# Optimization experiments

Hardware: AMD Instinct MI355X
Metric: run time of the kernel (lower is better)

## Reference

```python
import jax, jax.numpy as jnp
import numpy as np

EMBED_DIM = 768
NUM_HEADS = 12
MAX_LEN = 512
BATCH = 8
SEQ = 512
HEAD_DIM = EMBED_DIM // NUM_HEADS


def setup_inputs() -> dict:
    key = jax.random.key(0)
    ks = jax.random.split(key, 7)
    x = jax.random.normal(ks[0], (BATCH, SEQ, EMBED_DIM), dtype=jnp.float32)
    mask = jnp.ones((BATCH, SEQ), dtype=jnp.int32)
    Wq = jax.random.normal(ks[1], (EMBED_DIM, EMBED_DIM), dtype=jnp.float32) * (1.0 / np.sqrt(EMBED_DIM))
    Wk = jax.random.normal(ks[2], (EMBED_DIM, EMBED_DIM), dtype=jnp.float32) * (1.0 / np.sqrt(EMBED_DIM))
    Wv = jax.random.normal(ks[3], (EMBED_DIM, EMBED_DIM), dtype=jnp.float32) * (1.0 / np.sqrt(EMBED_DIM))
    rel_pos = jax.random.normal(ks[4], (2 * MAX_LEN - 1, NUM_HEADS), dtype=jnp.float32)
    Wo = jax.random.normal(ks[5], (EMBED_DIM, EMBED_DIM), dtype=jnp.float32) * (1.0 / np.sqrt(EMBED_DIM))
    bo = jax.random.normal(ks[6], (EMBED_DIM,), dtype=jnp.float32) * 0.02
    return {"x": x, "mask": mask, "Wq": Wq, "Wk": Wk, "Wv": Wv,
            "rel_pos": rel_pos, "Wo": Wo, "bo": bo}


def reference(x, mask, Wq, Wk, Wv, rel_pos, Wo, bo):
    B, S, E = x.shape
    H, D = NUM_HEADS, HEAD_DIM
    Q = (x @ Wq).reshape(B, S, H, D)
    K = (x @ Wk).reshape(B, S, H, D)
    V = (x @ Wv).reshape(B, S, H, D)
    # scores: [B, H, S, S]
    scores = jnp.einsum('bqhd,bkhd->bhqk', Q, K) / np.sqrt(D).astype(np.float32)
    # relative position bias: idx[q,k] = k - q + max_len - 1, clamped
    pos = jnp.arange(S)
    idx = jnp.clip(pos[None, :] - pos[:, None] + MAX_LEN - 1, 0, 2 * MAX_LEN - 2)
    bias = rel_pos[idx]                       # [S, S, H]
    scores = scores + jnp.transpose(bias, (2, 0, 1))[None]  # [1,H,S,S]
    # mask: b i * b j -> [B,1,S,S]
    m2 = (mask[:, None, :, None] * mask[:, None, None, :]) != 0
    mask_value = -jnp.finfo(scores.dtype).max
    scores = jnp.where(m2, scores, mask_value)
    attn = jax.nn.softmax(scores, axis=-1)
    out = jnp.einsum('bhqk,bkhd->bqhd', attn, V).reshape(B, S, E)
    out = out @ Wo + bo  # dropout is identity in eval mode
    return out
```

## Files before the change

kernel.cpp:

```cpp
#include <hip/hip_runtime.h>
#include <hip/hip_bf16.h>
#include <cfloat>
#include <cstdint>
#include <cmath>

#define EMBED 768
#define NHEAD 12
#define SEQB  8
#define SEQ   512
#define HDIM  64
#define WMAT  589824

typedef __attribute__((ext_vector_type(8))) short short8;
typedef __attribute__((ext_vector_type(4))) short short4v;
typedef __attribute__((ext_vector_type(4))) float f32x4;

__device__ __forceinline__ short f2bf(float f) {
  uint32_t u = __float_as_uint(f);
  u += 0x7FFF + ((u >> 16) & 1u);
  return (short)(u >> 16);
}

__device__ __forceinline__ short f2bf1(float f) {
  int r;
  asm("v_cvt_pk_bf16_f32 %0, %1, %2" : "=v"(r) : "v"(f), "v"(f));
  return (short)r;
}

__device__ __forceinline__ void gload_lds16(const void* g, void* l) {
  __builtin_amdgcn_global_load_lds((const __attribute__((address_space(1))) void*)g,
                                   (__attribute__((address_space(3))) void*)l, 16, 0, 0);
}

__global__ void k_cast_x(const float* __restrict__ x, short* __restrict__ xb) {
  int i = blockIdx.x * blockDim.x + threadIdx.x;
  const int n4 = SEQB * SEQ * EMBED / 4;
  if (i < n4) {
    float4 v = ((const float4*)x)[i];
    short4v o;
    o.x = f2bf(v.x); o.y = f2bf(v.y); o.z = f2bf(v.z); o.w = f2bf(v.w);
    ((short4v*)xb)[i] = o;
  }
}

__global__ void k_cast_wt(const float* __restrict__ Wq, const float* __restrict__ Wk,
                          const float* __restrict__ Wv, const float* __restrict__ Wo,
                          short* __restrict__ Wt) {
  __shared__ float tile[32][33];
  const int mat = blockIdx.z;
  const float* src = (mat == 0) ? Wq : (mat == 1) ? Wk : (mat == 2) ? Wv : Wo;
  const int n0 = blockIdx.x * 32, k0 = blockIdx.y * 32;
  const int tx = threadIdx.x & 31, ty = threadIdx.x >> 5;
  #pragma unroll
  for (int rr = 0; rr < 4; rr++)
    tile[ty + rr * 8][tx] = src[(size_t)(k0 + ty + rr * 8) * EMBED + n0 + tx];
  __syncthreads();
  short* dst = Wt + (size_t)mat * WMAT;
  #pragma unroll
  for (int rr = 0; rr < 4; rr++)
    dst[(size_t)(n0 + ty + rr * 8) * EMBED + k0 + tx] = f2bf(tile[tx][ty + rr * 8]);
}

template <int MODE>
__launch_bounds__(256)
__global__ void k_gemm(const short* __restrict__ A, const short* __restrict__ B,
                       short* __restrict__ O0, short* __restrict__ O1,
                       short* __restrict__ O2,
                       float* __restrict__ OF, const float* __restrict__ bias) {
  __shared__ __attribute__((aligned(16))) short As[2][128 * 32];
  __shared__ __attribute__((aligned(16))) short Bs[2][128 * 32];
  const int tid = threadIdx.x;
  const int lane = tid & 63, w = tid >> 6;
  const int g = lane >> 4, c = lane & 15;
  const int wi = (w >> 1) * 64, wj = (w & 1) * 64;
  const int i0 = blockIdx.y * 128, j0 = blockIdx.x * 128;
  const int NSTEP = EMBED / 32;

  f32x4 acc[4][4];
  #pragma unroll
  for (int a = 0; a < 4; a++)
    #pragma unroll
    for (int b2 = 0; b2 < 4; b2++) acc[a][b2] = (f32x4){0.f, 0.f, 0.f, 0.f};

  #define GSTAGE(S, BUF)                                                            \
    { _Pragma("unroll")                                                             \
      for (int it = 0; it < 2; it++) {                                              \
        int gi = tid + it * 256;                                                    \
        int row = gi >> 2, qq = gi & 3;                                             \
        gload_lds16(A + (size_t)(i0 + row) * EMBED + (S) * 32 + qq * 8,             \
                    &As[BUF][gi * 8]);                                              \
        gload_lds16(B + (size_t)(j0 + row) * EMBED + (S) * 32 + qq * 8,             \
                    &Bs[BUF][gi * 8]);                                              \
      } }

  GSTAGE(0, 0)
  __syncthreads();

  for (int s = 0; s < NSTEP; ++s) {
    const int cur = s & 1;
    if (s < NSTEP - 1) {
      GSTAGE(s + 1, cur ^ 1)
      asm volatile("s_waitcnt vmcnt(4)" ::: "memory");
    } else {
      asm volatile("s_waitcnt vmcnt(0)" ::: "memory");
    }
    __builtin_amdgcn_sched_barrier(0);
    __builtin_amdgcn_s_barrier();
    __builtin_amdgcn_sched_barrier(0);

    short8 aF[4], bF[4];
    #pragma unroll
    for (int mi = 0; mi < 4; mi++) aF[mi] = *(const short8*)&As[cur][(wi + mi * 16 + c) * 32 + g * 8];
    #pragma unroll
    for (int nj = 0; nj < 4; nj++) bF[nj] = *(const short8*)&Bs[cur][(wj + nj * 16 + c) * 32 + g * 8];
    #pragma unroll
    for (int mi = 0; mi < 4; mi++)
      #pragma unroll
      for (int nj = 0; nj < 4; nj++)
        acc[mi][nj] = __builtin_amdgcn_mfma_f32_16x16x32_bf16(aF[mi], bF[nj], acc[mi][nj], 0, 0, 0);

    __builtin_amdgcn_s_barrier();
    __builtin_amdgcn_sched_barrier(0);
  }

  #pragma unroll
  for (int mi = 0; mi < 4; mi++) {
    int i = i0 + wi + mi * 16 + 4 * g;
    #pragma unroll
    for (int nj = 0; nj < 4; nj++) {
      int j = j0 + wj + nj * 16 + c;
      f32x4 v = acc[mi][nj];
      if (MODE == 0) {
        int n = i, m = j;
        int b = m >> 9, s = m & 511;
        if (n < 1536) {
          short* dst = O0; int nn = n;
          if (n >= 768) { dst = O1; nn -= 768; }
          int h = nn >> 6, d = nn & 63;
          short4v o; o.x = f2bf(v.x); o.y = f2bf(v.y); o.z = f2bf(v.z); o.w = f2bf(v.w);
          *(short4v*)&dst[(size_t)(((b * 12 + h) * 512 + s) * 64 + d)] = o;
        } else {
          int nn = n - 1536;
          int h = nn >> 6, d = nn & 63;
          size_t base = ((size_t)(b * 12 + h) * 64 + d) * 512 + s;
          O2[base] = f2bf(v.x); O2[base + 512] = f2bf(v.y);
          O2[base + 1024] = f2bf(v.z); O2[base + 1536] = f2bf(v.w);
        }
      } else {
        int n = i, m = j;
        float4 bb = *(const float4*)&bias[n];
        float4 o; o.x = v.x + bb.x; o.y = v.y + bb.y; o.z = v.z + bb.z; o.w = v.w + bb.w;
        *(float4*)&OF[(size_t)m * EMBED + n] = o;
      }
    }
  }
}

__launch_bounds__(256)
__global__ void k_attn(const short* __restrict__ Q, const short* __restrict__ K,
                       const short* __restrict__ Vt, const int* __restrict__ mask,
                       const float* __restrict__ rel_pos, short* __restrict__ attO) {
  __shared__ float bias_lds[1024];
  __shared__ int mask_lds[512];
  __shared__ __attribute__((aligned(16))) short Plds[4][16 * 32];
  __shared__ __attribute__((aligned(16))) short Kbuf[2][32 * 64];
  __shared__ __attribute__((aligned(16))) short Vbuf[2][64 * 32];
  const int tid = threadIdx.x;
  const int lane = tid & 63, w = tid >> 6;
  const int g = lane >> 4, c = lane & 15;
  const int bid = blockIdx.x;
  const int q0 = (bid / 96) * 64;
  const int bh = bid % 96;
  const int b = bh / 12, h = bh % 12;
  const short* Qb = Q + (size_t)bh * (512 * 64);
  const short* Kb = K + (size_t)bh * (512 * 64);
  const short* Vb = Vt + (size_t)bh * (64 * 512);

  const float LOG2E = 1.44269504089f;
  for (int i = tid; i < 1023; i += 256) bias_lds[i] = (rel_pos[i * 12 + h] - 16.0f) * LOG2E;
  for (int i = tid; i < 512; i += 256) mask_lds[i] = mask[b * 512 + i];

  const int krow_s = tid >> 3, kc_s = tid & 7;
  const int vrow_s = tid >> 2, vc_s = tid & 3;
  #define STAGEKV(T, BUF)                                                             \
    {                                                                                 \
      gload_lds16(Kb + ((T) * 32 + krow_s) * 64 + (kc_s ^ (krow_s & 7)) * 8,          \
                  &Kbuf[BUF][tid * 8]);                                               \
      gload_lds16(Vb + (size_t)vrow_s * 512 + (T) * 32 + (vc_s ^ ((vrow_s >> 1) & 3)) * 8, \
                  &Vbuf[BUF][tid * 8]);                                               \
    }

  STAGEKV(0, 0)

  short8 qf[2];
  #pragma unroll
  for (int dc = 0; dc < 2; dc++)
    qf[dc] = *(const short8*)&Qb[(q0 + w * 16 + c) * 64 + dc * 32 + g * 8];

  __syncthreads();

  int qrow[4], mq[4], bbase[4];
  #pragma unroll
  for (int r = 0; r < 4; r++) {
    qrow[r] = q0 + w * 16 + 4 * g + r;
    mq[r] = mask_lds[qrow[r]];
    bbase[r] = 511 - qrow[r];
  }

  float l_part[4];
  f32x4 accO[4];
  #pragma unroll
  for (int r = 0; r < 4; r++) l_part[r] = 0.f;
  #pragma unroll
  for (int dt = 0; dt < 4; dt++) accO[dt] = (f32x4){0.f, 0.f, 0.f, 0.f};

  const float SC = 0.125f * 1.44269504089f;
  short* Pw = &Plds[w][0];
  const int rdoff = c * 32 + g * 8;
  const int kswz = c & 7;
  const int vswz = (c >> 1) & 3;

  for (int t = 0; t < 16; ++t) {
    const int cur = t & 1;
    if (t < 15) {
      STAGEKV(t + 1, cur ^ 1)
      asm volatile("s_waitcnt vmcnt(2)" ::: "memory");
    } else {
      asm volatile("s_waitcnt vmcnt(0)" ::: "memory");
    }
    __builtin_amdgcn_sched_barrier(0);
    __builtin_amdgcn_s_barrier();
    __builtin_amdgcn_sched_barrier(0);

    const short* Kt = &Kbuf[cur][0];
    const short* Vs = &Vbuf[cur][0];

    short8 kf[4], vf[4];
    #pragma unroll
    for (int ct = 0; ct < 2; ct++)
      #pragma unroll
      for (int dc = 0; dc < 2; dc++)
        kf[ct * 2 + dc] = *(const short8*)&Kt[(ct * 16 + c) * 64 + ((dc * 4 + g) ^ kswz) * 8];
    #pragma unroll
    for (int dt = 0; dt < 4; dt++)
      vf[dt] = *(const short8*)&Vs[(dt * 16 + c) * 32 + ((g ^ vswz)) * 8];

    f32x4 s0 = (f32x4){0.f, 0.f, 0.f, 0.f}, s1 = s0;
    s0 = __builtin_amdgcn_mfma_f32_16x16x32_bf16(qf[0], kf[0], s0, 0, 0, 0);
    s0 = __builtin_amdgcn_mfma_f32_16x16x32_bf16(qf[1], kf[1], s0, 0, 0, 0);
    s1 = __builtin_amdgcn_mfma_f32_16x16x32_bf16(qf[0], kf[2], s1, 0, 0, 0);
    s1 = __builtin_amdgcn_mfma_f32_16x16x32_bf16(qf[1], kf[3], s1, 0, 0, 0);

    float p_[2][4];
    {
      const int krow = t * 32 + c;
      const int mk0 = mask_lds[krow], mk1 = mask_lds[krow + 16];
      #pragma unroll
      for (int r = 0; r < 4; r++) {
        float a0 = fmaf(s0[r], SC, bias_lds[krow + bbase[r]]);
        float a1 = fmaf(s1[r], SC, bias_lds[krow + 16 + bbase[r]]);
        float p0 = exp2f(a0), p1 = exp2f(a1);
        if ((mq[r] & mk0) == 0) p0 = 0.f;
        if ((mq[r] & mk1) == 0) p1 = 0.f;
        p_[0][r] = p0; p_[1][r] = p1;
        l_part[r] += p0 + p1;
      }
    }
    #pragma unroll
    for (int ct = 0; ct < 2; ct++)
      #pragma unroll
      for (int r = 0; r < 4; r++)
        Pw[(4 * g + r) * 32 + ct * 16 + c] = f2bf1(p_[ct][r]);
    short8 pa = *(const short8*)&Pw[rdoff];
    #pragma unroll
    for (int dt = 0; dt < 4; dt++)
      accO[dt] = __builtin_amdgcn_mfma_f32_16x16x32_bf16(pa, vf[dt], accO[dt], 0, 0, 0);

    __builtin_amdgcn_s_barrier();
    __builtin_amdgcn_sched_barrier(0);
  }

  float inv[4];
  #pragma unroll
  for (int r = 0; r < 4; r++) {
    float lr = l_part[r];
    #pragma unroll
    for (int off = 1; off < 16; off <<= 1) lr += __shfl_xor(lr, off);
    inv[r] = 1.0f / lr;
  }
  #pragma unroll
  for (int dt = 0; dt < 4; dt++)
    #pragma unroll
    for (int r = 0; r < 4; r++)
      attO[(size_t)(b * 512 + qrow[r]) * EMBED + h * 64 + dt * 16 + c] =
          f2bf(accO[dt][r] * inv[r]);
}

extern "C" void kernel_launch(void* const* d_in, const int* in_sizes, int n_in,
                              void* d_out, int out_size, void* d_ws, size_t ws_size,
                              hipStream_t stream) {
  const float* x = (const float*)d_in[0];
  const int* mask = (const int*)d_in[1];
  const float* Wq = (const float*)d_in[2];
  const float* Wk = (const float*)d_in[3];
  const float* Wv = (const float*)d_in[4];
  const float* rel_pos = (const float*)d_in[5];
  const float* Wo = (const float*)d_in[6];
  const float* bo = (const float*)d_in[7];
  float* out = (float*)d_out;

  char* ws = (char*)d_ws;
  short* xb = (short*)ws;
  short* Wt = (short*)(ws + 6291456);
  short* Qg = (short*)(ws + 6291456 + 4718592);
  short* Kg = Qg + 3145728;
  short* Vt = Kg + 3145728;
  short* attO = xb;

  k_cast_x<<<3072, 256, 0, stream>>>(x, xb);
  k_cast_wt<<<dim3(24, 24, 4), 256, 0, stream>>>(Wq, Wk, Wv, Wo, Wt);
  k_gemm<0><<<dim3(32, 18), 256, 0, stream>>>(Wt, xb, Qg, Kg, Vt, nullptr, nullptr);
  k_attn<<<768, 256, 0, stream>>>(Qg, Kg, Vt, mask, rel_pos, attO);
  k_gemm<2><<<dim3(32, 6), 256, 0, stream>>>(Wt + 3 * WMAT, attO, nullptr, nullptr, nullptr, out, bo);
}
```

Before: 155.6 us.

## Fuse cast kernels, triple-buffer GEMM stages, widen attention KV tiles

```diff
diff --git a/kernel.cpp b/kernel.cpp
--- a/kernel.cpp
+++ b/kernel.cpp
@@ -32,33 +32,32 @@
                                    (__attribute__((address_space(3))) void*)l, 16, 0, 0);
 }
 
-__global__ void k_cast_x(const float* __restrict__ x, short* __restrict__ xb) {
-  int i = blockIdx.x * blockDim.x + threadIdx.x;
-  const int n4 = SEQB * SEQ * EMBED / 4;
-  if (i < n4) {
+__global__ void k_cast(const float* __restrict__ x,
+                       const float* __restrict__ Wq, const float* __restrict__ Wk,
+                       const float* __restrict__ Wv, const float* __restrict__ Wo,
+                       short* __restrict__ xb, short* __restrict__ Wt) {
+  __shared__ float tile[32][33];
+  const int bx = blockIdx.x;
+  if (bx < 2304) {
+    const int mat = bx / 576, rem = bx % 576;
+    const float* src = (mat == 0) ? Wq : (mat == 1) ? Wk : (mat == 2) ? Wv : Wo;
+    const int n0 = (rem % 24) * 32, k0 = (rem / 24) * 32;
+    const int tx = threadIdx.x & 31, ty = threadIdx.x >> 5;
+    #pragma unroll
+    for (int rr = 0; rr < 4; rr++)
+      tile[ty + rr * 8][tx] = src[(size_t)(k0 + ty + rr * 8) * EMBED + n0 + tx];
+    __syncthreads();
+    short* dst = Wt + (size_t)mat * WMAT;
+    #pragma unroll
+    for (int rr = 0; rr < 4; rr++)
+      dst[(size_t)(n0 + ty + rr * 8) * EMBED + k0 + tx] = f2bf(tile[tx][ty + rr * 8]);
+  } else {
+    int i = (bx - 2304) * 256 + threadIdx.x;
     float4 v = ((const float4*)x)[i];
     short4v o;
     o.x = f2bf(v.x); o.y = f2bf(v.y); o.z = f2bf(v.z); o.w = f2bf(v.w);
     ((short4v*)xb)[i] = o;
   }
-}
-
-__global__ void k_cast_wt(const float* __restrict__ Wq, const float* __restrict__ Wk,
-                          const float* __restrict__ Wv, const float* __restrict__ Wo,
-                          short* __restrict__ Wt) {
-  __shared__ float tile[32][33];
-  const int mat = blockIdx.z;
-  const float* src = (mat == 0) ? Wq : (mat == 1) ? Wk : (mat == 2) ? Wv : Wo;
-  const int n0 = blockIdx.x * 32, k0 = blockIdx.y * 32;
-  const int tx = threadIdx.x & 31, ty = threadIdx.x >> 5;
-  #pragma unroll
-  for (int rr = 0; rr < 4; rr++)
-    tile[ty + rr * 8][tx] = src[(size_t)(k0 + ty + rr * 8) * EMBED + n0 + tx];
-  __syncthreads();
-  short* dst = Wt + (size_t)mat * WMAT;
-  #pragma unroll
-  for (int rr = 0; rr < 4; rr++)
-    dst[(size_t)(n0 + ty + rr * 8) * EMBED + k0 + tx] = f2bf(tile[tx][ty + rr * 8]);
 }
 
 template <int MODE>
@@ -67,8 +66,8 @@
                        short* __restrict__ O0, short* __restrict__ O1,
                        short* __restrict__ O2,
                        float* __restrict__ OF, const float* __restrict__ bias) {
-  __shared__ __attribute__((aligned(16))) short As[2][128 * 32];
-  __shared__ __attribute__((aligned(16))) short Bs[2][128 * 32];
+  __shared__ __attribute__((aligned(16))) short As[3][128 * 32];
+  __shared__ __attribute__((aligned(16))) short Bs[3][128 * 32];
   const int tid = threadIdx.x;
   const int lane = tid & 63, w = tid >> 6;
   const int g = lane >> 4, c = lane & 15;
@@ -94,12 +93,14 @@
       } }
 
   GSTAGE(0, 0)
-  __syncthreads();
+  GSTAGE(1, 1)
 
   for (int s = 0; s < NSTEP; ++s) {
-    const int cur = s & 1;
-    if (s < NSTEP - 1) {
-      GSTAGE(s + 1, cur ^ 1)
+    const int cur = s % 3;
+    if (s + 2 < NSTEP) {
+      GSTAGE(s + 2, (s + 2) % 3)
+      asm volatile("s_waitcnt vmcnt(8)" ::: "memory");
+    } else if (s + 1 < NSTEP) {
       asm volatile("s_waitcnt vmcnt(4)" ::: "memory");
     } else {
       asm volatile("s_waitcnt vmcnt(0)" ::: "memory");
@@ -162,9 +163,9 @@
                        const float* __restrict__ rel_pos, short* __restrict__ attO) {
   __shared__ float bias_lds[1024];
   __shared__ int mask_lds[512];
-  __shared__ __attribute__((aligned(16))) short Plds[4][16 * 32];
-  __shared__ __attribute__((aligned(16))) short Kbuf[2][32 * 64];
-  __shared__ __attribute__((aligned(16))) short Vbuf[2][64 * 32];
+  __shared__ __attribute__((aligned(16))) short Plds[4][16 * 64];
+  __shared__ __attribute__((aligned(16))) short Kbuf[2][64 * 64];
+  __shared__ __attribute__((aligned(16))) short Vbuf[2][64 * 64];
   const int tid = threadIdx.x;
   const int lane = tid & 63, w = tid >> 6;
   const int g = lane >> 4, c = lane & 15;
@@ -180,15 +181,16 @@
   for (int i = tid; i < 1023; i += 256) bias_lds[i] = (rel_pos[i * 12 + h] - 16.0f) * LOG2E;
   for (int i = tid; i < 512; i += 256) mask_lds[i] = mask[b * 512 + i];
 
-  const int krow_s = tid >> 3, kc_s = tid & 7;
-  const int vrow_s = tid >> 2, vc_s = tid & 3;
   #define STAGEKV(T, BUF)                                                             \
-    {                                                                                 \
-      gload_lds16(Kb + ((T) * 32 + krow_s) * 64 + (kc_s ^ (krow_s & 7)) * 8,          \
-                  &Kbuf[BUF][tid * 8]);                                               \
-      gload_lds16(Vb + (size_t)vrow_s * 512 + (T) * 32 + (vc_s ^ ((vrow_s >> 1) & 3)) * 8, \
-                  &Vbuf[BUF][tid * 8]);                                               \
-    }
+    { _Pragma("unroll")                                                               \
+      for (int it = 0; it < 2; it++) {                                                \
+        int gi = tid + it * 256;                                                      \
+        int row = gi >> 3, ch = gi & 7;                                               \
+        gload_lds16(Kb + ((T) * 64 + row) * 64 + (ch ^ (row & 7)) * 8,                \
+                    &Kbuf[BUF][gi * 8]);                                              \
+        gload_lds16(Vb + (size_t)row * 512 + (T) * 64 + (ch ^ (row & 7)) * 8,         \
+                    &Vbuf[BUF][gi * 8]);                                              \
+      } }
 
   STAGEKV(0, 0)
 
@@ -216,15 +218,13 @@
 
   const float SC = 0.125f * 1.44269504089f;
   short* Pw = &Plds[w][0];
-  const int rdoff = c * 32 + g * 8;
-  const int kswz = c & 7;
-  const int vswz = (c >> 1) & 3;
-
-  for (int t = 0; t < 16; ++t) {
+  const int cswz = c & 7;
+
+  for (int t = 0; t < 8; ++t) {
     const int cur = t & 1;
-    if (t < 15) {
+    if (t < 7) {
       STAGEKV(t + 1, cur ^ 1)
-      asm volatile("s_waitcnt vmcnt(2)" ::: "memory");
+      asm volatile("s_waitcnt vmcnt(4)" ::: "memory");
     } else {
       asm volatile("s_waitcnt vmcnt(0)" ::: "memory");
     }
@@ -235,46 +235,44 @@
     const short* Kt = &Kbuf[cur][0];
     const short* Vs = &Vbuf[cur][0];
 
-    short8 kf[4], vf[4];
-    #pragma unroll
-    for (int ct = 0; ct < 2; ct++)
-      #pragma unroll
-      for (int dc = 0; dc < 2; dc++)
-        kf[ct * 2 + dc] = *(const short8*)&Kt[(ct * 16 + c) * 64 + ((dc * 4 + g) ^ kswz) * 8];
-    #pragma unroll
-    for (int dt = 0; dt < 4; dt++)
-      vf[dt] = *(const short8*)&Vs[(dt * 16 + c) * 32 + ((g ^ vswz)) * 8];
-
-    f32x4 s0 = (f32x4){0.f, 0.f, 0.f, 0.f}, s1 = s0;
-    s0 = __builtin_amdgcn_mfma_f32_16x16x32_bf16(qf[0], kf[0], s0, 0, 0, 0);
-    s0 = __builtin_amdgcn_mfma_f32_16x16x32_bf16(qf[1], kf[1], s0, 0, 0, 0);
-    s1 = __builtin_amdgcn_mfma_f32_16x16x32_bf16(qf[0], kf[2], s1, 0, 0, 0);
-    s1 = __builtin_amdgcn_mfma_f32_16x16x32_bf16(qf[1], kf[3], s1, 0, 0, 0);
-
-    float p_[2][4];
-    {
-      const int krow = t * 32 + c;
-      const int mk0 = mask_lds[krow], mk1 = mask_lds[krow + 16];
+    f32x4 s4[4];
+    #pragma unroll
+    for (int ct = 0; ct < 4; ct++) {
+      short8 kf0 = *(const short8*)&Kt[(ct * 16 + c) * 64 + ((0 + g) ^ cswz) * 8];
+      short8 kf1 = *(const short8*)&Kt[(ct * 16 + c) * 64 + ((4 + g) ^ cswz) * 8];
+      f32x4 s = (f32x4){0.f, 0.f, 0.f, 0.f};
+      s = __builtin_amdgcn_mfma_f32_16x16x32_bf16(qf[0], kf0, s, 0, 0, 0);
+      s = __builtin_amdgcn_mfma_f32_16x16x32_bf16(qf[1], kf1, s, 0, 0, 0);
+      s4[ct] = s;
+    }
+
+    #pragma unroll
+    for (int ct = 0; ct < 4; ct++) {
+      const int krow = t * 64 + ct * 16 + c;
+      const int mk = mask_lds[krow];
+      float p_[4];
       #pragma unroll
       for (int r = 0; r < 4; r++) {
-        float a0 = fmaf(s0[r], SC, bias_lds[krow + bbase[r]]);
-        float a1 = fmaf(s1[r], SC, bias_lds[krow + 16 + bbase[r]]);
-        float p0 = exp2f(a0), p1 = exp2f(a1);
-        if ((mq[r] & mk0) == 0) p0 = 0.f;
-        if ((mq[r] & mk1) == 0) p1 = 0.f;
-        p_[0][r] = p0; p_[1][r] = p1;
-        l_part[r] += p0 + p1;
+        float a0 = fmaf(s4[ct][r], SC, bias_lds[krow + bbase[r]]);
+        float pv = exp2f(a0);
+        if ((mq[r] & mk) == 0) pv = 0.f;
+        p_[r] = pv;
+        l_part[r] += pv;
       }
-    }
-    #pragma unroll
-    for (int ct = 0; ct < 2; ct++)
       #pragma unroll
       for (int r = 0; r < 4; r++)
-        Pw[(4 * g + r) * 32 + ct * 16 + c] = f2bf1(p_[ct][r]);
-    short8 pa = *(const short8*)&Pw[rdoff];
-    #pragma unroll
-    for (int dt = 0; dt < 4; dt++)
-      accO[dt] = __builtin_amdgcn_mfma_f32_16x16x32_bf16(pa, vf[dt], accO[dt], 0, 0, 0);
+        Pw[(4 * g + r) * 64 + ct * 16 + c] = f2bf1(p_[r]);
+    }
+
+    short8 pa0 = *(const short8*)&Pw[c * 64 + g * 8];
+    short8 pa1 = *(const short8*)&Pw[c * 64 + 32 + g * 8];
+    #pragma unroll
+    for (int dt = 0; dt < 4; dt++) {
+      short8 vf0 = *(const short8*)&Vs[(dt * 16 + c) * 64 + ((0 + g) ^ cswz) * 8];
+      short8 vf1 = *(const short8*)&Vs[(dt * 16 + c) * 64 + ((4 + g) ^ cswz) * 8];
+      accO[dt] = __builtin_amdgcn_mfma_f32_16x16x32_bf16(pa0, vf0, accO[dt], 0, 0, 0);
+      accO[dt] = __builtin_amdgcn_mfma_f32_16x16x32_bf16(pa1, vf1, accO[dt], 0, 0, 0);
+    }
 
     __builtin_amdgcn_s_barrier();
     __builtin_amdgcn_sched_barrier(0);
@@ -317,8 +315,7 @@
   short* Vt = Kg + 3145728;
   short* attO = xb;
 
-  k_cast_x<<<3072, 256, 0, stream>>>(x, xb);
-  k_cast_wt<<<dim3(24, 24, 4), 256, 0, stream>>>(Wq, Wk, Wv, Wo, Wt);
+  k_cast<<<5376, 256, 0, stream>>>(x, Wq, Wk, Wv, Wo, xb, Wt);
   k_gemm<0><<<dim3(32, 18), 256, 0, stream>>>(Wt, xb, Qg, Kg, Vt, nullptr, nullptr);
   k_attn<<<768, 256, 0, stream>>>(Qg, Kg, Vt, mask, rel_pos, attO);
   k_gemm<2><<<dim3(32, 6), 256, 0, stream>>>(Wt + 3 * WMAT, attO, nullptr, nullptr, nullptr, out, bo);
```

Result: faster. 149.5 us (-3.9%).
